# Performance work log

Hardware: AMD Instinct MI355X
Metric: run time of the kernel (lower is better)

Reference implementation:

```python
import jax, jax.numpy as jnp
import numpy as np
from jax.scipy.special import logsumexp

T, B, D, L = 1024, 32, 768, 48
NEG = jnp.float32(-1e20)


def setup_inputs() -> dict:
    key = jax.random.key(0)
    ks = jax.random.split(key, 10)
    feats = jax.random.normal(ks[0], (T, B, D), jnp.float32)
    # tags: True = label disallowed at this position (partial annotation mask)
    tags = jax.random.uniform(ks[1], (T, B, L)) < 0.3
    lens = jax.random.randint(ks[2], (B,), T // 2, T + 1)
    W = jax.random.normal(ks[3], (D, L), jnp.float32) * 0.02
    b = jnp.zeros((L,), jnp.float32)
    base = jnp.float32(1.0 / L)
    begin_transition = jnp.full((L,), base) + 0.01 * jax.random.normal(ks[4], (L,), jnp.float32)
    transitions = jnp.full((L, L), base) + 0.01 * jax.random.normal(ks[5], (L, L), jnp.float32)
    end_transition = jnp.full((L,), base) + 0.01 * jax.random.normal(ks[6], (L,), jnp.float32)
    begin_constraints = jax.random.uniform(ks[7], (L,)) < 0.2
    end_constraints = jax.random.uniform(ks[8], (L,)) < 0.2
    transition_constraints = jax.random.uniform(ks[9], (L, L)) < 0.2
    return {
        "feats": feats, "tags": tags, "lens": lens,
        "W": W, "b": b,
        "begin_transition": begin_transition, "transitions": transitions,
        "end_transition": end_transition,
        "begin_constraints": begin_constraints, "end_constraints": end_constraints,
        "transition_constraints": transition_constraints,
    }


def _crf_logZ(emissions, begin, trans, end, tag_mask, lens):
    """Forward algorithm over [T,B,L] emissions; tag_mask True = disallowed.
    Returns log partition per batch element, read out at step lens-1."""
    fs0 = emissions[0] + begin[None, :]              # [B, L]
    fs0 = jnp.where(tag_mask[0], NEG, fs0)

    def step(prev, xs):
        em_t, m_t = xs
        # new[b, j] = logsumexp_k(prev[b, k] + trans[j, k]) + em_t[b, j]
        new = logsumexp(prev[:, None, :] + trans[None, :, :], axis=-1) + em_t
        new = jnp.where(m_t, NEG, new)
        return new, new

    _, ys = jax.lax.scan(step, fs0, (emissions[1:], tag_mask[1:]))
    all_fs = jnp.concatenate([fs0[None], ys], axis=0)        # [T, B, L]
    last = all_fs[lens - 1, jnp.arange(lens.shape[0])]       # [B, L]
    return logsumexp(last + end[None, :], axis=-1)           # [B]


def reference(feats, tags, lens, W, b, begin_transition, transitions,
              end_transition, begin_constraints, end_constraints,
              transition_constraints):
    # feature2labels (Dropout is identity in eval)
    emissions = jnp.einsum('tbd,dl->tbl', feats, W) + b      # [T, B, L]
    no_mask = jnp.zeros_like(tags)

    # forward_alg: unconstrained partition function
    fwd = _crf_logZ(emissions, begin_transition, transitions,
                    end_transition, no_mask, lens)

    # partial_score: constrained params + gold tag masking
    begin_m = jnp.where(begin_constraints, NEG, begin_transition)
    trans_m = jnp.where(transition_constraints, NEG, transitions)
    end_m = jnp.where(end_constraints, NEG, end_transition)
    par = _crf_logZ(emissions, begin_m, trans_m, end_m, tags, lens)

    # criterion per batch element (sum over batch = original scalar loss)
    return fwd - par                                          # [B]
```

## Files before the change

kernel.cpp:

```cpp
#include <hip/hip_runtime.h>

#define T_ 1024
#define B_ 32
#define D_ 768
#define L_ 48
#define TB_ (T_ * B_)

__global__ __launch_bounds__(256) void emis_gemm(
    const float* __restrict__ feats, const float* __restrict__ W,
    const float* __restrict__ bias, float* __restrict__ E) {
  __shared__ float fbuf[128 * 68];
  __shared__ float wbuf[48 * 68];
  const int tid = threadIdx.x;
  const int cg = tid & 7;
  const int rg = tid >> 3;
  const int c0 = cg * 6;
  const int r0 = rg * 4;
  const int rowbase = blockIdx.x * 128;

  float acc[4][6];
#pragma unroll
  for (int i = 0; i < 4; i++)
#pragma unroll
    for (int c = 0; c < 6; c++) acc[i][c] = 0.f;

  float4 freg[8];
  float wreg[12];

  auto load_chunk = [&](int kc) {
#pragma unroll
    for (int i = 0; i < 8; i++) {
      int flat = i * 1024 + tid * 4;
      int r = flat >> 6;
      int kp = flat & 63;
      freg[i] = *(const float4*)(feats + (size_t)(rowbase + r) * D_ + kc + kp);
    }
#pragma unroll
    for (int i = 0; i < 12; i++) {
      int idx = tid + i * 256;
      int ko = idx / 48;
      int j = idx - ko * 48;
      wreg[i] = W[(kc + ko) * L_ + j];
    }
  };
  auto store_chunk = [&]() {
#pragma unroll
    for (int i = 0; i < 8; i++) {
      int flat = i * 1024 + tid * 4;
      int r = flat >> 6;
      int kp = flat & 63;
      *(float4*)(fbuf + r * 68 + kp) = freg[i];
    }
#pragma unroll
    for (int i = 0; i < 12; i++) {
      int idx = tid + i * 256;
      int ko = idx / 48;
      int j = idx - ko * 48;
      wbuf[j * 68 + ko] = wreg[i];
    }
  };

  load_chunk(0);
  for (int kc = 0; kc < D_; kc += 64) {
    __syncthreads();
    store_chunk();
    __syncthreads();
    if (kc + 64 < D_) load_chunk(kc + 64);
#pragma unroll 4
    for (int k4 = 0; k4 < 16; k4++) {
      float4 fv[4];
      float4 wv[6];
#pragma unroll
      for (int i = 0; i < 4; i++)
        fv[i] = *(const float4*)(fbuf + (r0 + i) * 68 + k4 * 4);
#pragma unroll
      for (int c = 0; c < 6; c++)
        wv[c] = *(const float4*)(wbuf + (c0 + c) * 68 + k4 * 4);
#pragma unroll
      for (int i = 0; i < 4; i++) {
#pragma unroll
        for (int c = 0; c < 6; c++) {
          acc[i][c] = fmaf(fv[i].x, wv[c].x, acc[i][c]);
          acc[i][c] = fmaf(fv[i].y, wv[c].y, acc[i][c]);
          acc[i][c] = fmaf(fv[i].z, wv[c].z, acc[i][c]);
          acc[i][c] = fmaf(fv[i].w, wv[c].w, acc[i][c]);
        }
      }
    }
  }
#pragma unroll
  for (int i = 0; i < 4; i++)
#pragma unroll
    for (int c = 0; c < 6; c++)
      E[(size_t)(rowbase + r0 + i) * L_ + c0 + c] =
          __expf(acc[i][c] + bias[c0 + c]);
}

__global__ __launch_bounds__(64) void crf_scan(
    const float* __restrict__ E, const int* __restrict__ tags,
    const int* __restrict__ lens, const float* __restrict__ begin,
    const float* __restrict__ trans, const float* __restrict__ endt,
    const int* __restrict__ bc, const int* __restrict__ ec,
    const int* __restrict__ tc, float* __restrict__ out) {
  const int s = blockIdx.x;
  const int pass = s & 1;
  const int b = s >> 1;
  const int lane = threadIdx.x;
  const bool act = lane < L_;
  const int len = lens[b];
  const int stride = B_ * L_;
  const int base = b * L_ + (act ? lane : 0);

  float P[L_];
#pragma unroll
  for (int k = 0; k < L_; k++) P[k] = 0.f;
  if (act) {
#pragma unroll
    for (int k = 0; k < L_; k++) {
      float p = __expf(trans[lane * L_ + k]);
      if (pass && tc[lane * L_ + k]) p = 0.f;
      P[k] = p;
    }
  }

  float a = 0.f;
  if (act) {
    a = E[base] * __expf(begin[lane]);
    if (pass && (bc[lane] || tags[base])) a = 0.f;
  }
  float logacc = 0.f;

  auto step = [&](float ev, int tg, bool rescale) {
    float s0 = 0.f, s1 = 0.f, s2 = 0.f, s3 = 0.f;
#pragma unroll
    for (int k = 0; k < L_; k += 4) {
      s0 = fmaf(__int_as_float(__builtin_amdgcn_readlane(__float_as_int(a), k + 0)), P[k + 0], s0);
      s1 = fmaf(__int_as_float(__builtin_amdgcn_readlane(__float_as_int(a), k + 1)), P[k + 1], s1);
      s2 = fmaf(__int_as_float(__builtin_amdgcn_readlane(__float_as_int(a), k + 2)), P[k + 2], s2);
      s3 = fmaf(__int_as_float(__builtin_amdgcn_readlane(__float_as_int(a), k + 3)), P[k + 3], s3);
    }
    float u = ((s0 + s1) + (s2 + s3)) * ev;
    if (pass && tg) u = 0.f;
    if (rescale) {
      float m = u;
#pragma unroll
      for (int off = 32; off; off >>= 1) m = fmaxf(m, __shfl_xor(m, off, 64));
      m = fmaxf(m, 1e-30f);
      u = u / m;
      logacc += __logf(m);
    }
    a = u;
  };

  float e8[8];
  int tg8[8];
#pragma unroll
  for (int i = 0; i < 8; i++) {
    int tt = 1 + i;
    e8[i] = E[tt * stride + base];
    tg8[i] = pass ? tags[tt * stride + base] : 0;
  }

  int t = 1;
  for (; t + 8 <= len; t += 8) {
    float p8[8];
    int q8[8];
#pragma unroll
    for (int i = 0; i < 8; i++) {
      int tt = t + 8 + i;
      tt = (tt < len) ? tt : (len - 1);
      p8[i] = E[tt * stride + base];
      q8[i] = pass ? tags[tt * stride + base] : 0;
    }
#pragma unroll
    for (int i = 0; i < 8; i++) step(e8[i], tg8[i], i == 7);
#pragma unroll
    for (int i = 0; i < 8; i++) { e8[i] = p8[i]; tg8[i] = q8[i]; }
  }
#pragma unroll
  for (int i = 0; i < 8; i++) {
    if (t + i < len) step(e8[i], tg8[i], false);
  }

  float z = 0.f;
  if (act) {
    float ez = __expf(endt[lane]);
    if (pass && ec[lane]) ez = 0.f;
    z = a * ez;
  }
#pragma unroll
  for (int off = 32; off; off >>= 1) z += __shfl_xor(z, off, 64);
  const float logZ = logacc + __logf(z);
  if (lane == 0) atomicAdd(out + b, pass ? -logZ : logZ);
}

extern "C" void kernel_launch(void* const* d_in, const int* in_sizes, int n_in,
                              void* d_out, int out_size, void* d_ws,
                              size_t ws_size, hipStream_t stream) {
  (void)in_sizes; (void)n_in; (void)out_size; (void)ws_size;
  const float* feats = (const float*)d_in[0];
  const int* tags = (const int*)d_in[1];
  const int* lens = (const int*)d_in[2];
  const float* W = (const float*)d_in[3];
  const float* bias = (const float*)d_in[4];
  const float* begin = (const float*)d_in[5];
  const float* trans = (const float*)d_in[6];
  const float* endt = (const float*)d_in[7];
  const int* bc = (const int*)d_in[8];
  const int* ec = (const int*)d_in[9];
  const int* tc = (const int*)d_in[10];

  float* E = (float*)d_ws;
  float* out = (float*)d_out;

  hipMemsetAsync(d_out, 0, B_ * sizeof(float), stream);

  emis_gemm<<<dim3(TB_ / 128), dim3(256), 0, stream>>>(feats, W, bias, E);
  crf_scan<<<dim3(2 * B_), dim3(64), 0, stream>>>(E, tags, lens, begin, trans,
                                                  endt, bc, ec, tc, out);
}
```

Before: 454.7 us.

## Load GEMM tiles directly to LDS with XOR swizzle; batch readlanes in scan

The emission GEMM now copies feature tiles straight from global memory into LDS with global_load_lds, using an XOR-swizzled unpadded layout in place of register staging and padding. The row mapping changes to interleaved rows (rg + 32*i), and outputs are written as float2. This drops the register double-buffering, so global-load latency is no longer overlapped with compute. The CRF scan hoists all 48 readlanes ahead of the FMA chain so the scalar reads can be issued back to back.

```diff
diff --git a/kernel.cpp b/kernel.cpp
--- a/kernel.cpp
+++ b/kernel.cpp
@@ -9,14 +9,16 @@
 __global__ __launch_bounds__(256) void emis_gemm(
     const float* __restrict__ feats, const float* __restrict__ W,
     const float* __restrict__ bias, float* __restrict__ E) {
-  __shared__ float fbuf[128 * 68];
+  __shared__ float fbuf[128 * 64];
   __shared__ float wbuf[48 * 68];
   const int tid = threadIdx.x;
+  const int wv = tid >> 6;
+  const int lane = tid & 63;
   const int cg = tid & 7;
   const int rg = tid >> 3;
   const int c0 = cg * 6;
-  const int r0 = rg * 4;
   const int rowbase = blockIdx.x * 128;
+  const int r7 = rg & 7;
 
   float acc[4][6];
 #pragma unroll
@@ -24,76 +26,67 @@
 #pragma unroll
     for (int c = 0; c < 6; c++) acc[i][c] = 0.f;
 
-  float4 freg[8];
-  float wreg[12];
-
-  auto load_chunk = [&](int kc) {
-#pragma unroll
-    for (int i = 0; i < 8; i++) {
-      int flat = i * 1024 + tid * 4;
-      int r = flat >> 6;
-      int kp = flat & 63;
-      freg[i] = *(const float4*)(feats + (size_t)(rowbase + r) * D_ + kc + kp);
-    }
-#pragma unroll
-    for (int i = 0; i < 12; i++) {
-      int idx = tid + i * 256;
-      int ko = idx / 48;
-      int j = idx - ko * 48;
-      wreg[i] = W[(kc + ko) * L_ + j];
-    }
-  };
-  auto store_chunk = [&]() {
-#pragma unroll
-    for (int i = 0; i < 8; i++) {
-      int flat = i * 1024 + tid * 4;
-      int r = flat >> 6;
-      int kp = flat & 63;
-      *(float4*)(fbuf + r * 68 + kp) = freg[i];
-    }
-#pragma unroll
-    for (int i = 0; i < 12; i++) {
-      int idx = tid + i * 256;
-      int ko = idx / 48;
-      int j = idx - ko * 48;
-      wbuf[j * 68 + ko] = wreg[i];
-    }
-  };
-
-  load_chunk(0);
   for (int kc = 0; kc < D_; kc += 64) {
     __syncthreads();
-    store_chunk();
+
+#pragma unroll
+    for (int inst = 0; inst < 8; inst++) {
+      const int rowstart = wv * 32 + inst * 4;
+      const int r = rowstart + (lane >> 4);
+      const int slot = lane & 15;
+      const int gch = slot ^ (r & 7);
+      const float* g = feats + (size_t)(rowbase + r) * D_ + kc + gch * 4;
+      float* l = fbuf + rowstart * 64;
+      __builtin_amdgcn_global_load_lds(
+          (const __attribute__((address_space(1))) uint32_t*)g,
+          (__attribute__((address_space(3))) uint32_t*)l, 16, 0, 0);
+    }
+
+#pragma unroll
+    for (int i = 0; i < 12; i++) {
+      const int idx = tid + i * 256;
+      const int ko = idx / 48;
+      const int j = idx - ko * 48;
+      wbuf[j * 68 + ko] = W[(kc + ko) * L_ + j];
+    }
+
     __syncthreads();
-    if (kc + 64 < D_) load_chunk(kc + 64);
+
 #pragma unroll 4
     for (int k4 = 0; k4 < 16; k4++) {
       float4 fv[4];
-      float4 wv[6];
+      float4 wv4[6];
+      const int sch = (k4 ^ r7) << 2;
 #pragma unroll
       for (int i = 0; i < 4; i++)
-        fv[i] = *(const float4*)(fbuf + (r0 + i) * 68 + k4 * 4);
+        fv[i] = *(const float4*)(fbuf + (rg + 32 * i) * 64 + sch);
 #pragma unroll
       for (int c = 0; c < 6; c++)
-        wv[c] = *(const float4*)(wbuf + (c0 + c) * 68 + k4 * 4);
+        wv4[c] = *(const float4*)(wbuf + (c0 + c) * 68 + k4 * 4);
 #pragma unroll
       for (int i = 0; i < 4; i++) {
 #pragma unroll
         for (int c = 0; c < 6; c++) {
-          acc[i][c] = fmaf(fv[i].x, wv[c].x, acc[i][c]);
-          acc[i][c] = fmaf(fv[i].y, wv[c].y, acc[i][c]);
-          acc[i][c] = fmaf(fv[i].z, wv[c].z, acc[i][c]);
-          acc[i][c] = fmaf(fv[i].w, wv[c].w, acc[i][c]);
+          acc[i][c] = fmaf(fv[i].x, wv4[c].x, acc[i][c]);
+          acc[i][c] = fmaf(fv[i].y, wv4[c].y, acc[i][c]);
+          acc[i][c] = fmaf(fv[i].z, wv4[c].z, acc[i][c]);
+          acc[i][c] = fmaf(fv[i].w, wv4[c].w, acc[i][c]);
         }
       }
     }
   }
-#pragma unroll
-  for (int i = 0; i < 4; i++)
-#pragma unroll
-    for (int c = 0; c < 6; c++)
-      E[(size_t)(rowbase + r0 + i) * L_ + c0 + c] =
-          __expf(acc[i][c] + bias[c0 + c]);
+
+#pragma unroll
+  for (int i = 0; i < 4; i++) {
+    float* dst = E + (size_t)(rowbase + rg + 32 * i) * L_ + c0;
+#pragma unroll
+    for (int c = 0; c < 6; c += 2) {
+      float2 v;
+      v.x = __expf(acc[i][c + 0] + bias[c0 + c + 0]);
+      v.y = __expf(acc[i][c + 1] + bias[c0 + c + 1]);
+      *(float2*)(dst + c) = v;
+    }
+  }
 }
 
 __global__ __launch_bounds__(64) void crf_scan(
@@ -131,13 +124,17 @@
   float logacc = 0.f;
 
   auto step = [&](float ev, int tg, bool rescale) {
+    const int ai = __float_as_int(a);
+    int sa[L_];
+#pragma unroll
+    for (int k = 0; k < L_; k++) sa[k] = __builtin_amdgcn_readlane(ai, k);
     float s0 = 0.f, s1 = 0.f, s2 = 0.f, s3 = 0.f;
 #pragma unroll
     for (int k = 0; k < L_; k += 4) {
-      s0 = fmaf(__int_as_float(__builtin_amdgcn_readlane(__float_as_int(a), k + 0)), P[k + 0], s0);
-      s1 = fmaf(__int_as_float(__builtin_amdgcn_readlane(__float_as_int(a), k + 1)), P[k + 1], s1);
-      s2 = fmaf(__int_as_float(__builtin_amdgcn_readlane(__float_as_int(a), k + 2)), P[k + 2], s2);
-      s3 = fmaf(__int_as_float(__builtin_amdgcn_readlane(__float_as_int(a), k + 3)), P[k + 3], s3);
+      s0 = fmaf(__int_as_float(sa[k + 0]), P[k + 0], s0);
+      s1 = fmaf(__int_as_float(sa[k + 1]), P[k + 1], s1);
+      s2 = fmaf(__int_as_float(sa[k + 2]), P[k + 2], s2);
+      s3 = fmaf(__int_as_float(sa[k + 3]), P[k + 3], s3);
     }
     float u = ((s0 + s1) + (s2 + s3)) * ev;
     if (pass && tg) u = 0.f;
@@ -156,9 +153,8 @@
   int tg8[8];
 #pragma unroll
   for (int i = 0; i < 8; i++) {
-    int tt = 1 + i;
-    e8[i] = E[tt * stride + base];
-    tg8[i] = pass ? tags[tt * stride + base] : 0;
+    e8[i] = E[(1 + i) * stride + base];
+    tg8[i] = pass ? tags[(1 + i) * stride + base] : 0;
   }
 
   int t = 1;
```

Measured after the change: 446.8 us. About the same (-1.7%).
